# Optimization experiments

Hardware: AMD Instinct MI355X
Metric: run time of the kernel (lower is better)

Reference implementation:

```python
import jax, jax.numpy as jnp
import numpy as np

HEADS = 4
DIM_HEAD = 32
SCALE = DIM_HEAD ** -0.5


def setup_inputs() -> dict:
    key = jax.random.key(0)
    k1, k2, k3 = jax.random.split(key, 3)
    dim = 128
    hidden = HEADS * DIM_HEAD  # 128
    x = jax.random.normal(k1, (4, dim, 64, 64), dtype=jnp.float32)
    w_qkv = jax.random.normal(k2, (3 * hidden, dim), dtype=jnp.float32) * (dim ** -0.5)
    w_out = jax.random.normal(k3, (dim, hidden), dtype=jnp.float32) * (hidden ** -0.5)
    b_out = jnp.zeros((dim,), dtype=jnp.float32)
    return {"x": x, "w_qkv": w_qkv, "w_out": w_out, "b_out": b_out}


def reference(x, w_qkv, w_out, b_out):
    b, c, h, w = x.shape
    n = h * w
    # 1x1 conv == channel matmul per pixel
    qkv = jnp.einsum('oc,bchw->bohw', w_qkv, x)  # [b, 3*hidden, h, w]
    q, k, v = jnp.split(qkv, 3, axis=1)
    # b (heads d) x y -> b heads d (x y)
    def to_heads(t):
        return t.reshape(b, HEADS, DIM_HEAD, n)
    q = to_heads(q) * SCALE
    k = to_heads(k)
    v = to_heads(v)
    sim = jnp.einsum('bhdi,bhdj->bhij', q, k)          # [b, heads, n, n]
    attn = jax.nn.softmax(sim, axis=-1)
    out = jnp.einsum('bhij,bhdj->bhid', attn, v)        # [b, heads, n, d]
    # b h (x y) d -> b (h d) x y
    out = out.transpose(0, 1, 3, 2).reshape(b, HEADS * DIM_HEAD, h, w)
    out = jnp.einsum('oc,bchw->bohw', w_out, out) + b_out[None, :, None, None]
    return out
```

## Files before the change

### kernel.cpp

```cpp
#include <hip/hip_runtime.h>
#include <math.h>

#define NHEAD 4
#define DHEAD 32
#define NPIX  4096
#define CIN   128
#define RP    8

typedef __bf16 bf16_t;
typedef __bf16 bf16x8 __attribute__((ext_vector_type(8)));
typedef __bf16 bf16x4 __attribute__((ext_vector_type(4)));
typedef float  f32x4  __attribute__((ext_vector_type(4)));

constexpr float QSCALE = 0.17677669529663687f * 1.4426950408889634f;

__global__ void __launch_bounds__(256) qkv_mfma(
    const float* __restrict__ x, const float* __restrict__ wqkv,
    ushort* __restrict__ qb, ushort* __restrict__ kb, ushort* __restrict__ vT) {
  __shared__ ushort Xls[32 * 136];
  const int blk = blockIdx.x, tid = threadIdx.x;
  const int half = blockIdx.y;
  const int wave = tid >> 6, lane = tid & 63;
  const int n = lane & 15, quad = lane >> 4;
  const int bb = blk >> 7;
  const int p0 = (blk & 127) * 32;

  {
    const int pc = tid & 7, c0 = (tid >> 3) * 4;
    const float* xp = x + ((size_t)bb * CIN + c0) * NPIX + p0 + pc * 4;
    float4 r0 = *(const float4*)xp;
    float4 r1 = *(const float4*)(xp + NPIX);
    float4 r2 = *(const float4*)(xp + 2 * NPIX);
    float4 r3 = *(const float4*)(xp + 3 * NPIX);
    bf16x4 w0 = {(bf16_t)r0.x, (bf16_t)r1.x, (bf16_t)r2.x, (bf16_t)r3.x};
    bf16x4 w1 = {(bf16_t)r0.y, (bf16_t)r1.y, (bf16_t)r2.y, (bf16_t)r3.y};
    bf16x4 w2 = {(bf16_t)r0.z, (bf16_t)r1.z, (bf16_t)r2.z, (bf16_t)r3.z};
    bf16x4 w3 = {(bf16_t)r0.w, (bf16_t)r1.w, (bf16_t)r2.w, (bf16_t)r3.w};
    *(bf16x4*)&Xls[(pc * 4 + 0) * 136 + c0] = w0;
    *(bf16x4*)&Xls[(pc * 4 + 1) * 136 + c0] = w1;
    *(bf16x4*)&Xls[(pc * 4 + 2) * 136 + c0] = w2;
    *(bf16x4*)&Xls[(pc * 4 + 3) * 136 + c0] = w3;
  }
  __syncthreads();

  bf16x8 xf[2][4];
#pragma unroll
  for (int nt = 0; nt < 2; ++nt)
#pragma unroll
    for (int k = 0; k < 4; ++k)
      xf[nt][k] = *(const bf16x8*)&Xls[(nt * 16 + n) * 136 + k * 32 + quad * 8];

#pragma unroll
  for (int mt = 0; mt < 3; ++mt) {
    const int ot = half * 12 + wave * 3 + mt;
    const int type = ot >> 3;
    const int wt = ot & 7, head = wt >> 1, d0 = (wt & 1) * 16;
    const int bh = bb * NHEAD + head;
    const float sc = (type == 0) ? QSCALE : 1.f;
    bf16x8 wf4[4];
#pragma unroll
    for (int k = 0; k < 4; ++k) {
      const float* ws = wqkv + (size_t)(ot * 16 + n) * CIN + k * 32 + quad * 8;
      float4 a = *(const float4*)ws;
      float4 b = *(const float4*)(ws + 4);
      wf4[k] = (bf16x8){(bf16_t)(a.x * sc), (bf16_t)(a.y * sc),
                        (bf16_t)(a.z * sc), (bf16_t)(a.w * sc),
                        (bf16_t)(b.x * sc), (bf16_t)(b.y * sc),
                        (bf16_t)(b.z * sc), (bf16_t)(b.w * sc)};
    }
    f32x4 acc[2] = {{0.f, 0.f, 0.f, 0.f}, {0.f, 0.f, 0.f, 0.f}};
    if (type < 2) {
#pragma unroll
      for (int k = 0; k < 4; ++k)
#pragma unroll
        for (int nt = 0; nt < 2; ++nt)
          acc[nt] = __builtin_amdgcn_mfma_f32_16x16x32_bf16(wf4[k], xf[nt][k], acc[nt], 0, 0, 0);
      ushort* dst = (type == 0) ? qb : kb;
#pragma unroll
      for (int nt = 0; nt < 2; ++nt) {
        bf16x4 o = {(bf16_t)acc[nt][0], (bf16_t)acc[nt][1],
                    (bf16_t)acc[nt][2], (bf16_t)acc[nt][3]};
        *(bf16x4*)(dst + ((size_t)bh * NPIX + p0 + nt * 16 + n) * DHEAD + d0 + quad * 4) = o;
      }
    } else {
#pragma unroll
      for (int k = 0; k < 4; ++k)
#pragma unroll
        for (int nt = 0; nt < 2; ++nt)
          acc[nt] = __builtin_amdgcn_mfma_f32_16x16x32_bf16(xf[nt][k], wf4[k], acc[nt], 0, 0, 0);
#pragma unroll
      for (int nt = 0; nt < 2; ++nt) {
        bf16x4 o = {(bf16_t)acc[nt][0], (bf16_t)acc[nt][1],
                    (bf16_t)acc[nt][2], (bf16_t)acc[nt][3]};
        *(bf16x4*)(vT + ((size_t)bh * DHEAD + d0 + n) * NPIX + p0 + nt * 16 + quad * 4) = o;
      }
    }
  }
}

__device__ __forceinline__ void ft_load(const ushort* kb0, const ushort* vb0,
                                        int t, bf16x8* kf, bf16x8* vf) {
#pragma unroll
  for (int p = 0; p < 2; ++p) {
#pragma unroll
    for (int s = 0; s < 2; ++s)
      kf[p * 2 + s] = *(const bf16x8*)(kb0 + (size_t)(t * 64 + p * 32 + s * 4) * DHEAD);
#pragma unroll
    for (int dp = 0; dp < 2; ++dp)
      vf[p * 2 + dp] = *(const bf16x8*)(vb0 + (size_t)dp * 16 * NPIX + t * 64 + p * 32);
  }
}

__device__ __forceinline__ void ft_compute(const bf16x8* qf, const bf16x8* kf,
                                           const bf16x8* vf, const bf16x8 ones,
                                           f32x4 O[RP][2], f32x4* Ol) {
  const f32x4 zero = {0.f, 0.f, 0.f, 0.f};
  __builtin_amdgcn_s_setprio(1);
#pragma unroll
  for (int p = 0; p < 2; ++p) {
#pragma unroll
    for (int rp = 0; rp < RP; ++rp) {
      f32x4 sa = __builtin_amdgcn_mfma_f32_16x16x32_bf16(kf[p * 2 + 0], qf[rp], zero, 0, 0, 0);
      f32x4 sb = __builtin_amdgcn_mfma_f32_16x16x32_bf16(kf[p * 2 + 1], qf[rp], zero, 0, 0, 0);
      bf16x8 pf;
#pragma unroll
      for (int r = 0; r < 4; ++r) {
        pf[r]     = (bf16_t)__builtin_amdgcn_exp2f(sa[r]);
        pf[r + 4] = (bf16_t)__builtin_amdgcn_exp2f(sb[r]);
      }
      O[rp][0] = __builtin_amdgcn_mfma_f32_16x16x32_bf16(pf, vf[p * 2 + 0], O[rp][0], 0, 0, 0);
      O[rp][1] = __builtin_amdgcn_mfma_f32_16x16x32_bf16(pf, vf[p * 2 + 1], O[rp][1], 0, 0, 0);
      Ol[rp]   = __builtin_amdgcn_mfma_f32_16x16x32_bf16(pf, ones, Ol[rp], 0, 0, 0);
    }
  }
  __builtin_amdgcn_s_setprio(0);
}

__global__ void __launch_bounds__(256, 2) flash_mfma(
    const ushort* __restrict__ qb, const ushort* __restrict__ kbuf,
    const ushort* __restrict__ vTb, ushort* __restrict__ ao) {
  __shared__ float Ols[4 * 128 * 36];
  const int tid = threadIdx.x, wave = tid >> 6, lane = tid & 63;
  const int n = lane & 15, quad = lane >> 4;

  const int id = blockIdx.x;
  const int bh = id & 15;
  const int qblk = id >> 4;
  const int js = wave;
  const int qrel = qblk * 128;

  const ushort* kg = kbuf + (size_t)bh * NPIX * DHEAD;
  const ushort* vg = vTb + (size_t)bh * DHEAD * NPIX;

  bf16x8 qf[RP];
#pragma unroll
  for (int rp = 0; rp < RP; ++rp)
    qf[rp] = *(const bf16x8*)(qb +
        ((size_t)bh * NPIX + qrel + rp * 16 + n) * DHEAD + quad * 8);

  f32x4 O[RP][2], Ol[RP];
#pragma unroll
  for (int rp = 0; rp < RP; ++rp) {
    O[rp][0] = (f32x4){0.f, 0.f, 0.f, 0.f};
    O[rp][1] = (f32x4){0.f, 0.f, 0.f, 0.f};
    Ol[rp]   = (f32x4){0.f, 0.f, 0.f, 0.f};
  }
  const bf16_t one = (bf16_t)1.0f;
  const bf16x8 ones = {one, one, one, one, one, one, one, one};

  const int pk = ((n >> 2) << 3) | (n & 3);
  const ushort* kb0 = kg + (size_t)(js * 1024 + pk) * DHEAD + quad * 8;
  const ushort* vb0 = vg + (size_t)n * NPIX + js * 1024 + quad * 8;

  bf16x8 kA[4], vA[4], kB[4], vB[4];
  ft_load(kb0, vb0, 0, kA, vA);
#pragma unroll 1
  for (int t = 0; t < 16; t += 2) {
    ft_load(kb0, vb0, t + 1, kB, vB);
    ft_compute(qf, kA, vA, ones, O, Ol);
    if (t + 2 < 16) ft_load(kb0, vb0, t + 2, kA, vA);
    ft_compute(qf, kB, vB, ones, O, Ol);
  }

  {
    float* pb = &Ols[wave * 128 * 36];
#pragma unroll
    for (int rp = 0; rp < RP; ++rp)
#pragma unroll
      for (int r = 0; r < 4; ++r) {
        const int q = rp * 16 + quad * 4 + r;
        pb[q * 36 + n]      = O[rp][0][r];
        pb[q * 36 + 16 + n] = O[rp][1][r];
        if (n == 0) pb[q * 36 + 32] = Ol[rp][r];
      }
  }
  __syncthreads();

  {
    const int q = tid >> 1, dh = tid & 1;
    f32x4 A0 = {0.f, 0.f, 0.f, 0.f}, A1 = A0, A2 = A0, A3 = A0;
    float l = 0.f;
#pragma unroll
    for (int w = 0; w < 4; ++w) {
      const float* pp = &Ols[(w * 128 + q) * 36 + dh * 16];
      A0 += *(const f32x4*)pp;
      A1 += *(const f32x4*)(pp + 4);
      A2 += *(const f32x4*)(pp + 8);
      A3 += *(const f32x4*)(pp + 12);
      l += pp[32 - dh * 16];
    }
    const float inv = 1.f / l;
    bf16x8 o0, o1;
#pragma unroll
    for (int e = 0; e < 4; ++e) {
      o0[e]     = (bf16_t)(A0[e] * inv);
      o0[e + 4] = (bf16_t)(A1[e] * inv);
      o1[e]     = (bf16_t)(A2[e] * inv);
      o1[e + 4] = (bf16_t)(A3[e] * inv);
    }
    ushort* dst = ao + ((size_t)((bh >> 2) * NPIX + qrel + q) * CIN
                        + (bh & 3) * 32 + dh * 16);
    *(bf16x8*)dst = o0;
    *(bf16x8*)(dst + 8) = o1;
  }
}

__global__ void __launch_bounds__(256) out_fused(
    const ushort* __restrict__ ao, const float* __restrict__ wout,
    const float* __restrict__ bias, float* __restrict__ out) {
  const int blk = blockIdx.x, tid = threadIdx.x;
  const int wave = tid >> 6, lane = tid & 63;
  const int n = lane & 15, quad = lane >> 4;
  const int bb = blk >> 8;
  const int p0 = (blk & 255) * 16;
  const int oc0 = wave * 32;

  bf16x8 wf[2][4];
#pragma unroll
  for (int mt = 0; mt < 2; ++mt)
#pragma unroll
    for (int k = 0; k < 4; ++k) {
      const float* ws = wout + (size_t)((wave * 2 + mt) * 16 + n) * CIN + k * 32 + quad * 8;
      float4 a = *(const float4*)ws;
      float4 b = *(const float4*)(ws + 4);
      wf[mt][k] = (bf16x8){(bf16_t)a.x, (bf16_t)a.y, (bf16_t)a.z, (bf16_t)a.w,
                           (bf16_t)b.x, (bf16_t)b.y, (bf16_t)b.z, (bf16_t)b.w};
    }

  bf16x8 bfr[4];
#pragma unroll
  for (int k = 0; k < 4; ++k)
    bfr[k] = *(const bf16x8*)(ao +
        ((size_t)(bb * NPIX + p0 + n) * CIN + k * 32 + quad * 8));

  f32x4 acc[2];
#pragma unroll
  for (int mt = 0; mt < 2; ++mt) acc[mt] = (f32x4){0.f, 0.f, 0.f, 0.f};
#pragma unroll
  for (int k = 0; k < 4; ++k)
#pragma unroll
    for (int mt = 0; mt < 2; ++mt)
      acc[mt] = __builtin_amdgcn_mfma_f32_16x16x32_bf16(
          wf[mt][k], bfr[k], acc[mt], 0, 0, 0);

#pragma unroll
  for (int mt = 0; mt < 2; ++mt) {
    const int oc = oc0 + mt * 16 + quad * 4;
#pragma unroll
    for (int r = 0; r < 4; ++r)
      out[((size_t)bb * CIN + oc + r) * NPIX + p0 + n] =
          acc[mt][r] + bias[oc + r];
  }
}

extern "C" void kernel_launch(void* const* d_in, const int* in_sizes, int n_in,
                              void* d_out, int out_size, void* d_ws, size_t ws_size,
                              hipStream_t stream) {
  const float* x     = (const float*)d_in[0];
  const float* w_qkv = (const float*)d_in[1];
  const float* w_out = (const float*)d_in[2];
  const float* b_out = (const float*)d_in[3];
  float* out = (float*)d_out;

  char* base = (char*)d_ws;
  ushort* qb = (ushort*)base;
  ushort* kb = (ushort*)(base + (size_t)4 * 1024 * 1024);
  ushort* vT = (ushort*)(base + (size_t)8 * 1024 * 1024);
  ushort* ao = (ushort*)(base + (size_t)12 * 1024 * 1024);

  qkv_mfma<<<dim3(512, 2), 256, 0, stream>>>(x, w_qkv, qb, kb, vT);
  flash_mfma<<<dim3(512), 256, 0, stream>>>(qb, kb, vT, ao);
  out_fused<<<dim3(1024), 256, 0, stream>>>(ao, w_out, b_out, out);
}
```

Before: 131.0 us.

## Fuse QKV, flash attention and output projection into one cooperative kernel

Replaces three separate kernel launches with a single cooperative kernel of 512 blocks that runs the QKV projection, attention, and output projection as phases separated by grid-wide syncs. Shared memory is unioned across phases. The aim is to remove launch overhead and inter-kernel gaps. In exchange, the QKV phase gets half as many blocks (each does 6 tiles instead of 3), the output phase gets 512 blocks instead of 1024, and grid syncs add cost. If the cooperative launch fails, it falls back to the original three launches.

```diff
diff --git a/kernel.cpp b/kernel.cpp
--- a/kernel.cpp
+++ b/kernel.cpp
@@ -1,4 +1,5 @@
 #include <hip/hip_runtime.h>
+#include <hip/hip_cooperative_groups.h>
 #include <math.h>
 
 #define NHEAD 4
@@ -12,7 +13,274 @@
 typedef __bf16 bf16x4 __attribute__((ext_vector_type(4)));
 typedef float  f32x4  __attribute__((ext_vector_type(4)));
 
+namespace cg = cooperative_groups;
+
 constexpr float QSCALE = 0.17677669529663687f * 1.4426950408889634f;
+
+__device__ __forceinline__ void ft_load(const ushort* kb0, const ushort* vb0,
+                                        int t, bf16x8* kf, bf16x8* vf) {
+#pragma unroll
+  for (int p = 0; p < 2; ++p) {
+#pragma unroll
+    for (int s = 0; s < 2; ++s)
+      kf[p * 2 + s] = *(const bf16x8*)(kb0 + (size_t)(t * 64 + p * 32 + s * 4) * DHEAD);
+#pragma unroll
+    for (int dp = 0; dp < 2; ++dp)
+      vf[p * 2 + dp] = *(const bf16x8*)(vb0 + (size_t)dp * 16 * NPIX + t * 64 + p * 32);
+  }
+}
+
+__device__ __forceinline__ void ft_compute(const bf16x8* qf, const bf16x8* kf,
+                                           const bf16x8* vf, const bf16x8 ones,
+                                           f32x4 O[RP][2], f32x4* Ol) {
+  const f32x4 zero = {0.f, 0.f, 0.f, 0.f};
+  __builtin_amdgcn_s_setprio(1);
+#pragma unroll
+  for (int p = 0; p < 2; ++p) {
+#pragma unroll
+    for (int rp = 0; rp < RP; ++rp) {
+      f32x4 sa = __builtin_amdgcn_mfma_f32_16x16x32_bf16(kf[p * 2 + 0], qf[rp], zero, 0, 0, 0);
+      f32x4 sb = __builtin_amdgcn_mfma_f32_16x16x32_bf16(kf[p * 2 + 1], qf[rp], zero, 0, 0, 0);
+      bf16x8 pf;
+#pragma unroll
+      for (int r = 0; r < 4; ++r) {
+        pf[r]     = (bf16_t)__builtin_amdgcn_exp2f(sa[r]);
+        pf[r + 4] = (bf16_t)__builtin_amdgcn_exp2f(sb[r]);
+      }
+      O[rp][0] = __builtin_amdgcn_mfma_f32_16x16x32_bf16(pf, vf[p * 2 + 0], O[rp][0], 0, 0, 0);
+      O[rp][1] = __builtin_amdgcn_mfma_f32_16x16x32_bf16(pf, vf[p * 2 + 1], O[rp][1], 0, 0, 0);
+      Ol[rp]   = __builtin_amdgcn_mfma_f32_16x16x32_bf16(pf, ones, Ol[rp], 0, 0, 0);
+    }
+  }
+  __builtin_amdgcn_s_setprio(0);
+}
+
+__device__ __forceinline__ void qkv_tiles(
+    const float* __restrict__ wqkv, const bf16x8 xf[2][4],
+    int ot_base, int mt_count, int bb, int p0, int lane, int n, int quad,
+    ushort* __restrict__ qb, ushort* __restrict__ kb, ushort* __restrict__ vT) {
+  for (int mt = 0; mt < mt_count; ++mt) {
+    const int ot = ot_base + mt;
+    const int type = ot >> 3;
+    const int wt = ot & 7, head = wt >> 1, d0 = (wt & 1) * 16;
+    const int bh = bb * NHEAD + head;
+    const float sc = (type == 0) ? QSCALE : 1.f;
+    bf16x8 wf4[4];
+#pragma unroll
+    for (int k = 0; k < 4; ++k) {
+      const float* ws = wqkv + (size_t)(ot * 16 + n) * CIN + k * 32 + quad * 8;
+      float4 a = *(const float4*)ws;
+      float4 b = *(const float4*)(ws + 4);
+      wf4[k] = (bf16x8){(bf16_t)(a.x * sc), (bf16_t)(a.y * sc),
+                        (bf16_t)(a.z * sc), (bf16_t)(a.w * sc),
+                        (bf16_t)(b.x * sc), (bf16_t)(b.y * sc),
+                        (bf16_t)(b.z * sc), (bf16_t)(b.w * sc)};
+    }
+    f32x4 acc[2] = {{0.f, 0.f, 0.f, 0.f}, {0.f, 0.f, 0.f, 0.f}};
+    if (type < 2) {
+#pragma unroll
+      for (int k = 0; k < 4; ++k)
+#pragma unroll
+        for (int nt = 0; nt < 2; ++nt)
+          acc[nt] = __builtin_amdgcn_mfma_f32_16x16x32_bf16(wf4[k], xf[nt][k], acc[nt], 0, 0, 0);
+      ushort* dst = (type == 0) ? qb : kb;
+#pragma unroll
+      for (int nt = 0; nt < 2; ++nt) {
+        bf16x4 o = {(bf16_t)acc[nt][0], (bf16_t)acc[nt][1],
+                    (bf16_t)acc[nt][2], (bf16_t)acc[nt][3]};
+        *(bf16x4*)(dst + ((size_t)bh * NPIX + p0 + nt * 16 + n) * DHEAD + d0 + quad * 4) = o;
+      }
+    } else {
+#pragma unroll
+      for (int k = 0; k < 4; ++k)
+#pragma unroll
+        for (int nt = 0; nt < 2; ++nt)
+          acc[nt] = __builtin_amdgcn_mfma_f32_16x16x32_bf16(xf[nt][k], wf4[k], acc[nt], 0, 0, 0);
+#pragma unroll
+      for (int nt = 0; nt < 2; ++nt) {
+        bf16x4 o = {(bf16_t)acc[nt][0], (bf16_t)acc[nt][1],
+                    (bf16_t)acc[nt][2], (bf16_t)acc[nt][3]};
+        *(bf16x4*)(vT + ((size_t)bh * DHEAD + d0 + n) * NPIX + p0 + nt * 16 + quad * 4) = o;
+      }
+    }
+  }
+}
+
+__global__ void __launch_bounds__(256, 2) fused_attn(
+    const float* __restrict__ x, const float* __restrict__ wqkv,
+    const float* __restrict__ wout, const float* __restrict__ bias,
+    ushort* __restrict__ qb, ushort* __restrict__ kb,
+    ushort* __restrict__ vT, ushort* __restrict__ ao,
+    float* __restrict__ out) {
+  __shared__ union {
+    ushort xls[32 * 136];
+    float  ols[4 * 128 * 36];
+  } sm;
+
+  const int tid = threadIdx.x, wave = tid >> 6, lane = tid & 63;
+  const int n = lane & 15, quad = lane >> 4;
+  const int blk = blockIdx.x;
+
+  {
+    const int bb = blk >> 7, p0 = (blk & 127) * 32;
+    {
+      const int pc = tid & 7, c0 = (tid >> 3) * 4;
+      const float* xp = x + ((size_t)bb * CIN + c0) * NPIX + p0 + pc * 4;
+      float4 r0 = *(const float4*)xp;
+      float4 r1 = *(const float4*)(xp + NPIX);
+      float4 r2 = *(const float4*)(xp + 2 * NPIX);
+      float4 r3 = *(const float4*)(xp + 3 * NPIX);
+      bf16x4 w0 = {(bf16_t)r0.x, (bf16_t)r1.x, (bf16_t)r2.x, (bf16_t)r3.x};
+      bf16x4 w1 = {(bf16_t)r0.y, (bf16_t)r1.y, (bf16_t)r2.y, (bf16_t)r3.y};
+      bf16x4 w2 = {(bf16_t)r0.z, (bf16_t)r1.z, (bf16_t)r2.z, (bf16_t)r3.z};
+      bf16x4 w3 = {(bf16_t)r0.w, (bf16_t)r1.w, (bf16_t)r2.w, (bf16_t)r3.w};
+      *(bf16x4*)&sm.xls[(pc * 4 + 0) * 136 + c0] = w0;
+      *(bf16x4*)&sm.xls[(pc * 4 + 1) * 136 + c0] = w1;
+      *(bf16x4*)&sm.xls[(pc * 4 + 2) * 136 + c0] = w2;
+      *(bf16x4*)&sm.xls[(pc * 4 + 3) * 136 + c0] = w3;
+    }
+    __syncthreads();
+    bf16x8 xf[2][4];
+#pragma unroll
+    for (int nt = 0; nt < 2; ++nt)
+#pragma unroll
+      for (int k = 0; k < 4; ++k)
+        xf[nt][k] = *(const bf16x8*)&sm.xls[(nt * 16 + n) * 136 + k * 32 + quad * 8];
+    qkv_tiles(wqkv, xf, wave * 6, 6, bb, p0, lane, n, quad, qb, kb, vT);
+  }
+
+  cg::this_grid().sync();
+
+  {
+    const int bh = blk & 15;
+    const int qblk = blk >> 4;
+    const int js = wave;
+    const int qrel = qblk * 128;
+
+    const ushort* kg = kb + (size_t)bh * NPIX * DHEAD;
+    const ushort* vg = vT + (size_t)bh * DHEAD * NPIX;
+
+    bf16x8 qf[RP];
+#pragma unroll
+    for (int rp = 0; rp < RP; ++rp)
+      qf[rp] = *(const bf16x8*)(qb +
+          ((size_t)bh * NPIX + qrel + rp * 16 + n) * DHEAD + quad * 8);
+
+    f32x4 O[RP][2], Ol[RP];
+#pragma unroll
+    for (int rp = 0; rp < RP; ++rp) {
+      O[rp][0] = (f32x4){0.f, 0.f, 0.f, 0.f};
+      O[rp][1] = (f32x4){0.f, 0.f, 0.f, 0.f};
+      Ol[rp]   = (f32x4){0.f, 0.f, 0.f, 0.f};
+    }
+    const bf16_t one = (bf16_t)1.0f;
+    const bf16x8 ones = {one, one, one, one, one, one, one, one};
+
+    const int pk = ((n >> 2) << 3) | (n & 3);
+    const ushort* kb0 = kg + (size_t)(js * 1024 + pk) * DHEAD + quad * 8;
+    const ushort* vb0 = vg + (size_t)n * NPIX + js * 1024 + quad * 8;
+
+    bf16x8 kA[4], vA[4], kB[4], vB[4];
+    ft_load(kb0, vb0, 0, kA, vA);
+#pragma unroll 1
+    for (int t = 0; t < 16; t += 2) {
+      ft_load(kb0, vb0, t + 1, kB, vB);
+      ft_compute(qf, kA, vA, ones, O, Ol);
+      if (t + 2 < 16) ft_load(kb0, vb0, t + 2, kA, vA);
+      ft_compute(qf, kB, vB, ones, O, Ol);
+    }
+
+    {
+      float* pb = &sm.ols[wave * 128 * 36];
+#pragma unroll
+      for (int rp = 0; rp < RP; ++rp)
+#pragma unroll
+        for (int r = 0; r < 4; ++r) {
+          const int q = rp * 16 + quad * 4 + r;
+          pb[q * 36 + n]      = O[rp][0][r];
+          pb[q * 36 + 16 + n] = O[rp][1][r];
+          if (n == 0) pb[q * 36 + 32] = Ol[rp][r];
+        }
+    }
+    __syncthreads();
+
+    {
+      const int q = tid >> 1, dh = tid & 1;
+      f32x4 A0 = {0.f, 0.f, 0.f, 0.f}, A1 = A0, A2 = A0, A3 = A0;
+      float l = 0.f;
+#pragma unroll
+      for (int w = 0; w < 4; ++w) {
+        const float* pp = &sm.ols[(w * 128 + q) * 36 + dh * 16];
+        A0 += *(const f32x4*)pp;
+        A1 += *(const f32x4*)(pp + 4);
+        A2 += *(const f32x4*)(pp + 8);
+        A3 += *(const f32x4*)(pp + 12);
+        l += pp[32 - dh * 16];
+      }
+      const float inv = 1.f / l;
+      bf16x8 o0, o1;
+#pragma unroll
+      for (int e = 0; e < 4; ++e) {
+        o0[e]     = (bf16_t)(A0[e] * inv);
+        o0[e + 4] = (bf16_t)(A1[e] * inv);
+        o1[e]     = (bf16_t)(A2[e] * inv);
+        o1[e + 4] = (bf16_t)(A3[e] * inv);
+      }
+      ushort* dst = ao + ((size_t)((bh >> 2) * NPIX + qrel + q) * CIN
+                          + (bh & 3) * 32 + dh * 16);
+      *(bf16x8*)dst = o0;
+      *(bf16x8*)(dst + 8) = o1;
+    }
+  }
+
+  cg::this_grid().sync();
+
+  {
+    const int bb = blk >> 7, base = (blk & 127) * 32;
+    const int oc0 = wave * 32;
+
+    bf16x8 wf[2][4];
+#pragma unroll
+    for (int mt = 0; mt < 2; ++mt)
+#pragma unroll
+      for (int k = 0; k < 4; ++k) {
+        const float* ws = wout + (size_t)((wave * 2 + mt) * 16 + n) * CIN + k * 32 + quad * 8;
+        float4 a = *(const float4*)ws;
+        float4 b = *(const float4*)(ws + 4);
+        wf[mt][k] = (bf16x8){(bf16_t)a.x, (bf16_t)a.y, (bf16_t)a.z, (bf16_t)a.w,
+                             (bf16_t)b.x, (bf16_t)b.y, (bf16_t)b.z, (bf16_t)b.w};
+      }
+
+#pragma unroll
+    for (int hh = 0; hh < 2; ++hh) {
+      const int p0 = base + hh * 16;
+      bf16x8 bfr[4];
+#pragma unroll
+      for (int k = 0; k < 4; ++k)
+        bfr[k] = *(const bf16x8*)(ao +
+            ((size_t)(bb * NPIX + p0 + n) * CIN + k * 32 + quad * 8));
+
+      f32x4 acc[2];
+#pragma unroll
+      for (int mt = 0; mt < 2; ++mt) acc[mt] = (f32x4){0.f, 0.f, 0.f, 0.f};
+#pragma unroll
+      for (int k = 0; k < 4; ++k)
+#pragma unroll
+        for (int mt = 0; mt < 2; ++mt)
+          acc[mt] = __builtin_amdgcn_mfma_f32_16x16x32_bf16(
+              wf[mt][k], bfr[k], acc[mt], 0, 0, 0);
+
+#pragma unroll
+      for (int mt = 0; mt < 2; ++mt) {
+        const int oc = oc0 + mt * 16 + quad * 4;
+#pragma unroll
+        for (int r = 0; r < 4; ++r)
+          out[((size_t)bb * CIN + oc + r) * NPIX + p0 + n] =
+              acc[mt][r] + bias[oc + r];
+      }
+    }
+  }
+}
 
 __global__ void __launch_bounds__(256) qkv_mfma(
     const float* __restrict__ x, const float* __restrict__ wqkv,
@@ -50,90 +318,7 @@
     for (int k = 0; k < 4; ++k)
       xf[nt][k] = *(const bf16x8*)&Xls[(nt * 16 + n) * 136 + k * 32 + quad * 8];
 
-#pragma unroll
-  for (int mt = 0; mt < 3; ++mt) {
-    const int ot = half * 12 + wave * 3 + mt;
-    const int type = ot >> 3;
-    const int wt = ot & 7, head = wt >> 1, d0 = (wt & 1) * 16;
-    const int bh = bb * NHEAD + head;
-    const float sc = (type == 0) ? QSCALE : 1.f;
-    bf16x8 wf4[4];
-#pragma unroll
-    for (int k = 0; k < 4; ++k) {
-      const float* ws = wqkv + (size_t)(ot * 16 + n) * CIN + k * 32 + quad * 8;
-      float4 a = *(const float4*)ws;
-      float4 b = *(const float4*)(ws + 4);
-      wf4[k] = (bf16x8){(bf16_t)(a.x * sc), (bf16_t)(a.y * sc),
-                        (bf16_t)(a.z * sc), (bf16_t)(a.w * sc),
-                        (bf16_t)(b.x * sc), (bf16_t)(b.y * sc),
-                        (bf16_t)(b.z * sc), (bf16_t)(b.w * sc)};
-    }
-    f32x4 acc[2] = {{0.f, 0.f, 0.f, 0.f}, {0.f, 0.f, 0.f, 0.f}};
-    if (type < 2) {
-#pragma unroll
-      for (int k = 0; k < 4; ++k)
-#pragma unroll
-        for (int nt = 0; nt < 2; ++nt)
-          acc[nt] = __builtin_amdgcn_mfma_f32_16x16x32_bf16(wf4[k], xf[nt][k], acc[nt], 0, 0, 0);
-      ushort* dst = (type == 0) ? qb : kb;
-#pragma unroll
-      for (int nt = 0; nt < 2; ++nt) {
-        bf16x4 o = {(bf16_t)acc[nt][0], (bf16_t)acc[nt][1],
-                    (bf16_t)acc[nt][2], (bf16_t)acc[nt][3]};
-        *(bf16x4*)(dst + ((size_t)bh * NPIX + p0 + nt * 16 + n) * DHEAD + d0 + quad * 4) = o;
-      }
-    } else {
-#pragma unroll
-      for (int k = 0; k < 4; ++k)
-#pragma unroll
-        for (int nt = 0; nt < 2; ++nt)
-          acc[nt] = __builtin_amdgcn_mfma_f32_16x16x32_bf16(xf[nt][k], wf4[k], acc[nt], 0, 0, 0);
-#pragma unroll
-      for (int nt = 0; nt < 2; ++nt) {
-        bf16x4 o = {(bf16_t)acc[nt][0], (bf16_t)acc[nt][1],
-                    (bf16_t)acc[nt][2], (bf16_t)acc[nt][3]};
-        *(bf16x4*)(vT + ((size_t)bh * DHEAD + d0 + n) * NPIX + p0 + nt * 16 + quad * 4) = o;
-      }
-    }
-  }
-}
-
-__device__ __forceinline__ void ft_load(const ushort* kb0, const ushort* vb0,
-                                        int t, bf16x8* kf, bf16x8* vf) {
-#pragma unroll
-  for (int p = 0; p < 2; ++p) {
-#pragma unroll
-    for (int s = 0; s < 2; ++s)
-      kf[p * 2 + s] = *(const bf16x8*)(kb0 + (size_t)(t * 64 + p * 32 + s * 4) * DHEAD);
-#pragma unroll
-    for (int dp = 0; dp < 2; ++dp)
-      vf[p * 2 + dp] = *(const bf16x8*)(vb0 + (size_t)dp * 16 * NPIX + t * 64 + p * 32);
-  }
-}
-
-__device__ __forceinline__ void ft_compute(const bf16x8* qf, const bf16x8* kf,
-                                           const bf16x8* vf, const bf16x8 ones,
-                                           f32x4 O[RP][2], f32x4* Ol) {
-  const f32x4 zero = {0.f, 0.f, 0.f, 0.f};
-  __builtin_amdgcn_s_setprio(1);
-#pragma unroll
-  for (int p = 0; p < 2; ++p) {
-#pragma unroll
-    for (int rp = 0; rp < RP; ++rp) {
-      f32x4 sa = __builtin_amdgcn_mfma_f32_16x16x32_bf16(kf[p * 2 + 0], qf[rp], zero, 0, 0, 0);
-      f32x4 sb = __builtin_amdgcn_mfma_f32_16x16x32_bf16(kf[p * 2 + 1], qf[rp], zero, 0, 0, 0);
-      bf16x8 pf;
-#pragma unroll
-      for (int r = 0; r < 4; ++r) {
-        pf[r]     = (bf16_t)__builtin_amdgcn_exp2f(sa[r]);
-        pf[r + 4] = (bf16_t)__builtin_amdgcn_exp2f(sb[r]);
-      }
-      O[rp][0] = __builtin_amdgcn_mfma_f32_16x16x32_bf16(pf, vf[p * 2 + 0], O[rp][0], 0, 0, 0);
-      O[rp][1] = __builtin_amdgcn_mfma_f32_16x16x32_bf16(pf, vf[p * 2 + 1], O[rp][1], 0, 0, 0);
-      Ol[rp]   = __builtin_amdgcn_mfma_f32_16x16x32_bf16(pf, ones, Ol[rp], 0, 0, 0);
-    }
-  }
-  __builtin_amdgcn_s_setprio(0);
+  qkv_tiles(wqkv, xf, half * 12 + wave * 3, 3, bb, p0, lane, n, quad, qb, kb, vT);
 }
 
 __global__ void __launch_bounds__(256, 2) flash_mfma(
@@ -288,7 +473,20 @@
   ushort* vT = (ushort*)(base + (size_t)8 * 1024 * 1024);
   ushort* ao = (ushort*)(base + (size_t)12 * 1024 * 1024);
 
-  qkv_mfma<<<dim3(512, 2), 256, 0, stream>>>(x, w_qkv, qb, kb, vT);
-  flash_mfma<<<dim3(512), 256, 0, stream>>>(qb, kb, vT, ao);
-  out_fused<<<dim3(1024), 256, 0, stream>>>(ao, w_out, b_out, out);
-}
+  const float* xa = x; const float* wqa = w_qkv;
+  const float* woa = w_out; const float* ba = b_out;
+  ushort* qba = qb; ushort* kba = kb; ushort* vta = vT; ushort* aoa = ao;
+  float* outa = out;
+  void* kargs[] = {(void*)&xa, (void*)&wqa, (void*)&woa, (void*)&ba,
+                   (void*)&qba, (void*)&kba, (void*)&vta, (void*)&aoa,
+                   (void*)&outa};
+
+  hipError_t err = hipLaunchCooperativeKernel(
+      (const void*)fused_attn, dim3(512), dim3(256), kargs, 0, stream);
+  if (err != hipSuccess) {
+    (void)hipGetLastError();
+    qkv_mfma<<<dim3(512, 2), 256, 0, stream>>>(x, w_qkv, qb, kb, vT);
+    flash_mfma<<<dim3(512), 256, 0, stream>>>(qb, kb, vT, ao);
+    out_fused<<<dim3(1024), 256, 0, stream>>>(ao, w_out, b_out, out);
+  }
+}
```

Result: slower. 245.5 us (+87.4%).
